# Optimization experiments

Hardware: AMD Instinct MI355X
Metric: run time of the kernel (lower is better)

Reference implementation:

```python
import jax, jax.numpy as jnp
import numpy as np


def setup_inputs() -> dict:
    key = jax.random.key(0)
    ks = jax.random.split(key, 5)
    B, IN, OUT = 8192, 4096, 4096
    in_q, out_q = IN // 4, OUT // 4
    # xavier-uniform-like scale for weights
    lim = float(np.sqrt(6.0 / (in_q + out_q)))
    return {
        "x": jax.random.normal(ks[0], (B, IN), dtype=jnp.float32),
        "Wa": jax.random.uniform(ks[1], (in_q, out_q), jnp.float32, -lim, lim),
        "Wb": jax.random.uniform(ks[2], (in_q, out_q), jnp.float32, -lim, lim),
        "Wc": jax.random.uniform(ks[3], (in_q, out_q), jnp.float32, -lim, lim),
        "Wd": jax.random.uniform(ks[4], (in_q, out_q), jnp.float32, -lim, lim),
        "bias": jnp.zeros((OUT,), dtype=jnp.float32),
    }


def reference(x, Wa, Wb, Wc, Wd, bias):
    # split quaternion components: [B, in_q] each
    a, b, c, d = jnp.split(x, 4, axis=1)
    # Hamilton product with weight quaternion (right multiplication)
    out_a = a @ Wa - b @ Wb - c @ Wc - d @ Wd
    out_b = a @ Wb + b @ Wa + c @ Wd - d @ Wc
    out_c = a @ Wc - b @ Wd + c @ Wa + d @ Wb
    out_d = a @ Wd + b @ Wc - c @ Wb + d @ Wa
    return jnp.concatenate([out_a, out_b, out_c, out_d], axis=1) + bias
```

## Files before the change

### kernel.cpp

```cpp
#include <hip/hip_runtime.h>
#include <hip/hip_bf16.h>
#include <cstdint>
#include <cstddef>

typedef __bf16 bf16_t;
typedef __bf16 bf16x4 __attribute__((ext_vector_type(4)));
typedef __bf16 bf16x8 __attribute__((ext_vector_type(8)));
typedef float f32x4 __attribute__((ext_vector_type(4)));

#define GLD16(src, dst)                                                       \
    __builtin_amdgcn_global_load_lds(                                         \
        (const __attribute__((address_space(1))) void*)(src),                 \
        (__attribute__((address_space(3))) void*)(dst), 16, 0, 0)

#define BAR() asm volatile("s_barrier" ::: "memory")
#define WAIT_VM4() asm volatile("s_waitcnt vmcnt(4)" ::: "memory")
#define WAIT_VM6() asm volatile("s_waitcnt vmcnt(6)" ::: "memory")
#define WAIT_VM0() asm volatile("s_waitcnt vmcnt(0)" ::: "memory")

__global__ __launch_bounds__(256) void cvt_x_kernel(const float* __restrict__ x,
                                                    bf16_t* __restrict__ xb, int n4) {
    int idx = blockIdx.x * blockDim.x + threadIdx.x;
    int stride = gridDim.x * blockDim.x;
    const f32x4* xv = (const f32x4*)x;
    bf16x4* ov = (bf16x4*)xb;
    for (int i = idx; i < n4; i += stride) {
        f32x4 v = xv[i];
        bf16x4 o;
        o[0] = (bf16_t)v[0];
        o[1] = (bf16_t)v[1];
        o[2] = (bf16_t)v[2];
        o[3] = (bf16_t)v[3];
        ov[i] = o;
    }
}

__global__ __launch_bounds__(256) void pack_w_kernel(const float* __restrict__ Wa,
                                                     const float* __restrict__ Wb,
                                                     const float* __restrict__ Wc,
                                                     const float* __restrict__ Wd,
                                                     bf16_t* __restrict__ Mt) {
    __shared__ float tile[64][65];
    const int kb = blockIdx.x * 64;
    const int nb = blockIdx.y * 64;
    const int i = kb >> 10;
    const int j = nb >> 10;

    const float* W[4] = {Wa, Wb, Wc, Wd};
    const int srcIdx[4][4] = {{0, 1, 2, 3}, {1, 0, 3, 2}, {2, 3, 0, 1}, {3, 2, 1, 0}};
    const float sgn[4][4] = {{1.f, 1.f, 1.f, 1.f},
                             {-1.f, 1.f, -1.f, 1.f},
                             {-1.f, 1.f, 1.f, -1.f},
                             {-1.f, -1.f, 1.f, 1.f}};
    const float* Ws = W[srcIdx[i][j]];
    const float s = sgn[i][j];

    const int kq = kb & 1023;
    const int nq = nb & 1023;
    const int tx = threadIdx.x & 63;
    const int ty = threadIdx.x >> 6;

    for (int r = ty; r < 64; r += 4)
        tile[r][tx] = Ws[(size_t)(kq + r) * 1024 + (nq + tx)];
    __syncthreads();
    for (int r = ty; r < 64; r += 4)
        Mt[(size_t)(nb + r) * 4096 + (kb + tx)] = (bf16_t)(s * tile[tx][r]);
}

__global__ __launch_bounds__(512, 2) void qgemm_kernel(const bf16_t* __restrict__ A,
                                                       const bf16_t* __restrict__ Bt,
                                                       const float* __restrict__ bias,
                                                       float* __restrict__ C) {
    constexpr int N = 4096, K = 4096;
    constexpr int NT = K / 64;
    extern __shared__ __align__(16) char lds[];

    const int tid = threadIdx.x;
    const int w = tid >> 6;
    const int lane = tid & 63;
    const int l15 = lane & 15, l4 = lane >> 4;
    const int wr = w >> 2, wc = w & 3;

    const int wg = blockIdx.x;
    const int swz = (wg & 7) * 64 + (wg >> 3);
    const int brow = (swz >> 4) * 256;
    const int bcol = (swz & 15) * 256;

    const int srow = lane >> 3;
    const int skb = (lane & 7) ^ (lane >> 3);

    auto stageA = [&](int buf, int h, int tt) {
#pragma unroll
        for (int q = 0; q < 2; ++q) {
            const bf16_t* src = A + (size_t)(brow + h * 128 + w * 16 + q * 8 + srow) * K +
                                tt * 64 + skb * 8;
            GLD16(src, lds + buf * 32768 + h * 16384 + w * 2048 + q * 1024);
        }
    };
    auto stageB = [&](int buf, int h, int tt) {
#pragma unroll
        for (int q = 0; q < 2; ++q) {
            const bf16_t* src = Bt + (size_t)(bcol + h * 128 + w * 16 + q * 8 + srow) * K +
                                tt * 64 + skb * 8;
            GLD16(src, lds + 65536 + buf * 32768 + h * 16384 + w * 2048 + q * 1024);
        }
    };

    f32x4 acc[8][4] = {};
    bf16x8 a[4][2], b0[2][2], b1[2][2];

    auto ldAm = [&](int buf, int mh, int m) {
#pragma unroll
        for (int c = 0; c < 2; ++c)
            a[m][c] = *(const bf16x8*)(lds + buf * 32768 + wr * 16384 +
                                       (mh * 64 + m * 16 + l15) * 128 +
                                       ((c * 4 + l4) ^ (l15 & 7)) * 16);
    };
    auto ldB = [&](int buf, int nh, bf16x8(&b)[2][2]) {
#pragma unroll
        for (int n = 0; n < 2; ++n)
#pragma unroll
            for (int c = 0; c < 2; ++c)
                b[n][c] = *(const bf16x8*)(lds + 65536 + buf * 32768 + nh * 16384 +
                                           (wc * 32 + n * 16 + l15) * 128 +
                                           ((c * 4 + l4) ^ (l15 & 7)) * 16);
    };
    auto mmac = [&](int mh, int nh, bf16x8(&b)[2][2]) {
        __builtin_amdgcn_s_setprio(1);
#pragma unroll
        for (int c = 0; c < 2; ++c)
#pragma unroll
            for (int m = 0; m < 4; ++m)
#pragma unroll
                for (int n = 0; n < 2; ++n)
                    acc[mh * 4 + m][nh * 2 + n] = __builtin_amdgcn_mfma_f32_16x16x32_bf16(
                        a[m][c], b[n][c], acc[mh * 4 + m][nh * 2 + n], 0, 0, 0);
        __builtin_amdgcn_s_setprio(0);
    };

#define TILE_BODY(CUR, TT)                                                    \
    {                                                                         \
        const int tt = (TT);                                                  \
                  \
        if (tt + 1 < NT) stageA((CUR) ^ 1, 1, tt + 1);                        \
        ldB((CUR), 1, b1);                                                    \
        mmac(0, 0, b0);                                                       \
        BAR();                                                                \
                          \
        if (tt + 2 < NT) stageB((CUR), 0, tt + 2);                            \
        mmac(0, 1, b1);                                                       \
        ldAm((CUR), 1, 0);                                                    \
        ldAm((CUR), 1, 1);                                                    \
        ldAm((CUR), 1, 2);                                                    \
        ldAm((CUR), 1, 3);                                                    \
        BAR();                                                                \
                 \
        if (tt + 2 < NT) stageB((CUR), 1, tt + 2);                            \
        mmac(1, 1, b1);                                                       \
        if (tt + 2 < NT) {                                                    \
            WAIT_VM4();                                                       \
        } else {                                                              \
            WAIT_VM0();                                                       \
        }                                                                     \
        BAR();                                                                \
                  \
        if (tt + 2 < NT) stageA((CUR), 0, tt + 2);                            \
        mmac(1, 0, b0);                                                       \
        if (tt + 1 < NT) {                                                    \
            ldB((CUR) ^ 1, 0, b0);                                            \
            ldAm((CUR) ^ 1, 0, 0);                                            \
            ldAm((CUR) ^ 1, 0, 1);                                            \
            ldAm((CUR) ^ 1, 0, 2);                                            \
            ldAm((CUR) ^ 1, 0, 3);                                            \
        }                                                                     \
        BAR();                                                                \
    }

    stageA(0, 0, 0);
    stageA(0, 1, 0);
    stageB(0, 0, 0);
    stageB(0, 1, 0);
    stageB(1, 0, 1);
    stageB(1, 1, 1);
    stageA(1, 0, 1);
    WAIT_VM6();
    BAR();
    ldB(0, 0, b0);
    ldAm(0, 0, 0);
    ldAm(0, 0, 1);
    ldAm(0, 0, 2);
    ldAm(0, 0, 3);

    for (int it = 0; it < NT / 2; ++it) {
        TILE_BODY(0, 2 * it);
        TILE_BODY(1, 2 * it + 1);
    }
#undef TILE_BODY

#pragma unroll
    for (int n = 0; n < 4; ++n) {
        const int col = bcol + (n >> 1) * 128 + wc * 32 + (n & 1) * 16 + l15;
        const float bv = bias[col];
#pragma unroll
        for (int m = 0; m < 8; ++m) {
            const int row0 = brow + wr * 128 + m * 16 + l4 * 4;
            const f32x4 v = acc[m][n];
#pragma unroll
            for (int i = 0; i < 4; ++i)
                C[(size_t)(row0 + i) * N + col] = v[i] + bv;
        }
    }
}

extern "C" void kernel_launch(void* const* d_in, const int* in_sizes, int n_in,
                              void* d_out, int out_size, void* d_ws, size_t ws_size,
                              hipStream_t stream) {
    const float* x = (const float*)d_in[0];
    const float* Wa = (const float*)d_in[1];
    const float* Wb = (const float*)d_in[2];
    const float* Wc = (const float*)d_in[3];
    const float* Wd = (const float*)d_in[4];
    const float* bias = (const float*)d_in[5];
    float* out = (float*)d_out;

    const int M = 8192, N = 4096, K = 4096;

    bf16_t* xb = (bf16_t*)d_ws;
    bf16_t* Mt = xb + (size_t)M * K;

    cvt_x_kernel<<<4096, 256, 0, stream>>>(x, xb, (M * K) / 4);
    pack_w_kernel<<<dim3(64, 64), 256, 0, stream>>>(Wa, Wb, Wc, Wd, Mt);

    (void)hipFuncSetAttribute((const void*)qgemm_kernel,
                              hipFuncAttributeMaxDynamicSharedMemorySize, 131072);
    qgemm_kernel<<<dim3((M / 256) * (N / 256)), 512, 131072, stream>>>(xb, Mt, bias, out);
}
```

Before: 276.0 us.

## Fuse fp32-to-bf16 conversion of x into GEMM A-tile staging

Removes the separate cvt_x kernel. The GEMM now loads fp32 x tiles into registers, converts them to bf16, and writes them to LDS itself, replacing the async global_load_lds path for A. This saves a full write and re-read of the bf16 copy of x, plus one kernel launch. In exchange, each A tile is read at twice the byte volume, and every CTA repeats the conversion across the 16 column blocks. It also adds register pressure and LDS write stalls (lgkmcnt waits) inside the main loop.

```diff
diff --git a/kernel.cpp b/kernel.cpp
--- a/kernel.cpp
+++ b/kernel.cpp
@@ -4,7 +4,6 @@
 #include <cstddef>
 
 typedef __bf16 bf16_t;
-typedef __bf16 bf16x4 __attribute__((ext_vector_type(4)));
 typedef __bf16 bf16x8 __attribute__((ext_vector_type(8)));
 typedef float f32x4 __attribute__((ext_vector_type(4)));
 
@@ -14,26 +13,7 @@
         (__attribute__((address_space(3))) void*)(dst), 16, 0, 0)
 
 #define BAR() asm volatile("s_barrier" ::: "memory")
-#define WAIT_VM4() asm volatile("s_waitcnt vmcnt(4)" ::: "memory")
-#define WAIT_VM6() asm volatile("s_waitcnt vmcnt(6)" ::: "memory")
-#define WAIT_VM0() asm volatile("s_waitcnt vmcnt(0)" ::: "memory")
-
-__global__ __launch_bounds__(256) void cvt_x_kernel(const float* __restrict__ x,
-                                                    bf16_t* __restrict__ xb, int n4) {
-    int idx = blockIdx.x * blockDim.x + threadIdx.x;
-    int stride = gridDim.x * blockDim.x;
-    const f32x4* xv = (const f32x4*)x;
-    bf16x4* ov = (bf16x4*)xb;
-    for (int i = idx; i < n4; i += stride) {
-        f32x4 v = xv[i];
-        bf16x4 o;
-        o[0] = (bf16_t)v[0];
-        o[1] = (bf16_t)v[1];
-        o[2] = (bf16_t)v[2];
-        o[3] = (bf16_t)v[3];
-        ov[i] = o;
-    }
-}
+#define LGKM0() asm volatile("s_waitcnt lgkmcnt(0)" ::: "memory")
 
 __global__ __launch_bounds__(256) void pack_w_kernel(const float* __restrict__ Wa,
                                                      const float* __restrict__ Wb,
@@ -67,7 +47,7 @@
         Mt[(size_t)(nb + r) * 4096 + (kb + tx)] = (bf16_t)(s * tile[tx][r]);
 }
 
-__global__ __launch_bounds__(512, 2) void qgemm_kernel(const bf16_t* __restrict__ A,
+__global__ __launch_bounds__(512, 2) void qgemm_kernel(const float* __restrict__ X,
                                                        const bf16_t* __restrict__ Bt,
                                                        const float* __restrict__ bias,
                                                        float* __restrict__ C) {
@@ -89,14 +69,6 @@
     const int srow = lane >> 3;
     const int skb = (lane & 7) ^ (lane >> 3);
 
-    auto stageA = [&](int buf, int h, int tt) {
-#pragma unroll
-        for (int q = 0; q < 2; ++q) {
-            const bf16_t* src = A + (size_t)(brow + h * 128 + w * 16 + q * 8 + srow) * K +
-                                tt * 64 + skb * 8;
-            GLD16(src, lds + buf * 32768 + h * 16384 + w * 2048 + q * 1024);
-        }
-    };
     auto stageB = [&](int buf, int h, int tt) {
 #pragma unroll
         for (int q = 0; q < 2; ++q) {
@@ -106,6 +78,30 @@
         }
     };
 
+    f32x4 rA0[4], rA1[4];
+
+    auto loadAf = [&](int h, int tt, f32x4(&r)[4]) {
+#pragma unroll
+        for (int q = 0; q < 2; ++q) {
+            const float* src = X + (size_t)(brow + h * 128 + w * 16 + q * 8 + srow) * K +
+                               tt * 64 + skb * 8;
+            r[q * 2 + 0] = *(const f32x4*)(src);
+            r[q * 2 + 1] = *(const f32x4*)(src + 4);
+        }
+    };
+    auto writeA = [&](int buf, int h, f32x4(&r)[4]) {
+#pragma unroll
+        for (int q = 0; q < 2; ++q) {
+            bf16x8 o;
+#pragma unroll
+            for (int j = 0; j < 4; ++j) {
+                o[j] = (bf16_t)r[q * 2 + 0][j];
+                o[4 + j] = (bf16_t)r[q * 2 + 1][j];
+            }
+            *(bf16x8*)(lds + buf * 32768 + h * 16384 + w * 2048 + q * 1024 + lane * 16) = o;
+        }
+    };
+
     f32x4 acc[8][4] = {};
     bf16x8 a[4][2], b0[2][2], b1[2][2];
 
@@ -141,30 +137,35 @@
 #define TILE_BODY(CUR, TT)                                                    \
     {                                                                         \
         const int tt = (TT);                                                  \
-                  \
-        if (tt + 1 < NT) stageA((CUR) ^ 1, 1, tt + 1);                        \
+                     \
+        if (tt + 1 < NT) {                                                    \
+            writeA((CUR) ^ 1, 1, rA1);                                        \
+            LGKM0();                                                          \
+        }                                                                     \
         ldB((CUR), 1, b1);                                                    \
         mmac(0, 0, b0);                                                       \
         BAR();                                                                \
-                          \
-        if (tt + 2 < NT) stageB((CUR), 0, tt + 2);                            \
+            \
+        if (tt + 2 < NT) {                                                    \
+            stageB((CUR), 0, tt + 2);                                         \
+            loadAf(0, tt + 2, rA0);                                           \
+        }                                                                     \
         mmac(0, 1, b1);                                                       \
         ldAm((CUR), 1, 0);                                                    \
         ldAm((CUR), 1, 1);                                                    \
         ldAm((CUR), 1, 2);                                                    \
         ldAm((CUR), 1, 3);                                                    \
         BAR();                                                                \
-                 \
+                                              \
         if (tt + 2 < NT) stageB((CUR), 1, tt + 2);                            \
         mmac(1, 1, b1);                                                       \
+        BAR();                                                                \
+                     \
         if (tt + 2 < NT) {                                                    \
-            WAIT_VM4();                                                       \
-        } else {                                                              \
-            WAIT_VM0();                                                       \
-        }                                                                     \
-        BAR();                                                                \
-                  \
-        if (tt + 2 < NT) stageA((CUR), 0, tt + 2);                            \
+            writeA((CUR), 0, rA0);                                            \
+            LGKM0();                                                          \
+            loadAf(1, tt + 2, rA1);                                           \
+        }                                                                     \
         mmac(1, 0, b0);                                                       \
         if (tt + 1 < NT) {                                                    \
             ldB((CUR) ^ 1, 0, b0);                                            \
@@ -176,14 +177,18 @@
         BAR();                                                                \
     }
 
-    stageA(0, 0, 0);
-    stageA(0, 1, 0);
     stageB(0, 0, 0);
     stageB(0, 1, 0);
+    loadAf(0, 0, rA0);
+    loadAf(1, 0, rA1);
     stageB(1, 0, 1);
     stageB(1, 1, 1);
-    stageA(1, 0, 1);
-    WAIT_VM6();
+    writeA(0, 0, rA0);
+    writeA(0, 1, rA1);
+    loadAf(0, 1, rA0);
+    writeA(1, 0, rA0);
+    loadAf(1, 1, rA1);
+    LGKM0();
     BAR();
     ldB(0, 0, b0);
     ldAm(0, 0, 0);
@@ -223,15 +228,13 @@
     const float* bias = (const float*)d_in[5];
     float* out = (float*)d_out;
 
-    const int M = 8192, N = 4096, K = 4096;
-
-    bf16_t* xb = (bf16_t*)d_ws;
-    bf16_t* Mt = xb + (size_t)M * K;
-
-    cvt_x_kernel<<<4096, 256, 0, stream>>>(x, xb, (M * K) / 4);
+    const int M = 8192, N = 4096;
+
+    bf16_t* Mt = (bf16_t*)d_ws;
+
     pack_w_kernel<<<dim3(64, 64), 256, 0, stream>>>(Wa, Wb, Wc, Wd, Mt);
 
     (void)hipFuncSetAttribute((const void*)qgemm_kernel,
                               hipFuncAttributeMaxDynamicSharedMemorySize, 131072);
-    qgemm_kernel<<<dim3((M / 256) * (N / 256)), 512, 131072, stream>>>(xb, Mt, bias, out);
+    qgemm_kernel<<<dim3((M / 256) * (N / 256)), 512, 131072, stream>>>(x, Mt, bias, out);
 }
```

Result: slower. 407.4 us (+47.6%).
